# Kernel optimization log

Hardware: AMD Instinct MI355X
Metric: run time of the kernel (lower is better)

The kernel has to match this reference:

```python
import jax, jax.numpy as jnp
import numpy as np

D_IN = 1024
D_OUT = 1024
NUM_HEADS = 16
HEAD_DIM = D_OUT // NUM_HEADS
SCALE = HEAD_DIM ** -0.5


def setup_inputs() -> dict:
    key = jax.random.key(0)
    k_x, k_qkv, k_pw, k_pb = jax.random.split(key, 4)
    B, S = 2, 2048
    x = jax.random.normal(k_x, (B, S, D_IN), dtype=jnp.float32)
    # nn.Linear weights: stored as (out_features, in_features); qkv_bias=False
    w_qkv = jax.random.normal(k_qkv, (3 * D_OUT, D_IN), dtype=jnp.float32) * (D_IN ** -0.5)
    w_proj = jax.random.normal(k_pw, (D_OUT, D_OUT), dtype=jnp.float32) * (D_OUT ** -0.5)
    b_proj = jax.random.normal(k_pb, (D_OUT,), dtype=jnp.float32) * 0.01
    return {"x": x, "w_qkv": w_qkv, "w_proj": w_proj, "b_proj": b_proj}


def reference(x, w_qkv, w_proj, b_proj):
    B, S, _ = x.shape
    # combined QKV projection: (B,S,3*d_out)
    qkv = jnp.einsum('bsd,ed->bse', x, w_qkv)
    qkv = qkv.reshape(B, S, 3, NUM_HEADS, HEAD_DIM)
    qkv = jnp.transpose(qkv, (2, 0, 3, 1, 4))  # (3,B,H,S,hd)
    q, k, v = qkv[0], qkv[1], qkv[2]
    scores = jnp.einsum('bhqd,bhkd->bhqk', q, k)  # (B,H,S,S)
    causal = jnp.triu(jnp.ones((S, S), dtype=bool), k=1)
    # module masks to -inf first, then scales (softmax-equivalent)
    scores = jnp.where(causal, -jnp.inf, scores) * SCALE
    attn = jax.nn.softmax(scores, axis=-1)
    ctx = jnp.einsum('bhqk,bhkd->bhqd', attn, v)
    ctx = jnp.transpose(ctx, (0, 2, 1, 3)).reshape(B, S, D_OUT)
    return jnp.einsum('bsd,ed->bse', ctx, w_proj) + b_proj
```

## Files before the change

kernel.cpp:

```cpp
#include <hip/hip_runtime.h>

#define SEQ    2048
#define NHEAD  16
#define HDIM   64
#define DMODEL 1024
#define BATCH  2

typedef __bf16 bf16;
typedef __bf16 bf16x8 __attribute__((ext_vector_type(8)));
typedef __bf16 bf16x4v __attribute__((ext_vector_type(4)));
typedef float  f32x4  __attribute__((ext_vector_type(4)));

typedef const __attribute__((address_space(1))) void* gas_ptr;
typedef __attribute__((address_space(3))) void*       las_ptr;

__device__ __forceinline__ f32x4 mfma16(bf16x8 a, bf16x8 b, f32x4 c) {
  return __builtin_amdgcn_mfma_f32_16x16x32_bf16(a, b, c, 0, 0, 0);
}

__device__ __forceinline__ void gload_lds16(const void* g, void* l) {
  __builtin_amdgcn_global_load_lds((gas_ptr)(unsigned long long)g,
                                   (las_ptr)(unsigned long long)l, 16, 0, 0);
}

__global__ void convert_all(const float* __restrict__ x, const float* __restrict__ wq,
                            const float* __restrict__ wp, bf16* __restrict__ out) {
  const long long NX = 4194304, NQ = 3145728, NP = 1048576;
  long long i = ((long long)blockIdx.x * blockDim.x + threadIdx.x) * 4;
  if (i >= NX + NQ + NP) return;
  const float* src; long long off;
  if (i < NX)           { src = x;  off = i; }
  else if (i < NX + NQ) { src = wq; off = i - NX; }
  else                  { src = wp; off = i - NX - NQ; }
  float4 f = *reinterpret_cast<const float4*>(src + off);
  bf16x4v r;
  r[0] = (bf16)f.x; r[1] = (bf16)f.y; r[2] = (bf16)f.z; r[3] = (bf16)f.w;
  *reinterpret_cast<bf16x4v*>(out + i) = r;
}

template <int EPI>
__global__ __launch_bounds__(256) void gemm_bt(
    const bf16* __restrict__ A, const bf16* __restrict__ B, int K,
    bf16* __restrict__ q, bf16* __restrict__ k, bf16* __restrict__ v,
    const float* __restrict__ bias, float* __restrict__ out) {
  __shared__ alignas(16) bf16 As[2][128 * 32];
  __shared__ alignas(16) bf16 Bs[2][128 * 32];

  const int tid = threadIdx.x;
  const int l = tid & 63, w = tid >> 6;
  const int lr = l & 15, lg = l >> 4;
  const int wr = (w >> 1) * 64, wc = (w & 1) * 64;
  const long long m0 = (long long)blockIdx.x * 128;
  const long long n0 = (long long)blockIdx.y * 128;
  const int crow = tid >> 2, ccol = (tid & 3) * 8;

  auto stage = [&](int kt, int buf) {
    const bf16* a_src = A + (m0 + crow) * K + (long long)kt * 32 + ccol;
    const bf16* b_src = B + (n0 + crow) * K + (long long)kt * 32 + ccol;
    gload_lds16(a_src,           &As[buf][tid * 8]);
    gload_lds16(a_src + 64LL * K, &As[buf][(tid + 256) * 8]);
    gload_lds16(b_src,           &Bs[buf][tid * 8]);
    gload_lds16(b_src + 64LL * K, &Bs[buf][(tid + 256) * 8]);
  };

  f32x4 acc[4][4];
  const f32x4 fz = {0.f, 0.f, 0.f, 0.f};
#pragma unroll
  for (int m = 0; m < 4; ++m)
#pragma unroll
    for (int n = 0; n < 4; ++n) acc[m][n] = fz;

  stage(0, 0);
  const int nk = K >> 5;
  int cur = 0;
  for (int kt = 0; kt < nk; ++kt) {
    __syncthreads();
    if (kt + 1 < nk) stage(kt + 1, cur ^ 1);
    bf16x8 af[4], bfv[4];
#pragma unroll
    for (int m = 0; m < 4; ++m)
      af[m] = *reinterpret_cast<const bf16x8*>(&As[cur][(wr + m * 16 + lr) * 32 + lg * 8]);
#pragma unroll
    for (int n = 0; n < 4; ++n)
      bfv[n] = *reinterpret_cast<const bf16x8*>(&Bs[cur][(wc + n * 16 + lr) * 32 + lg * 8]);
#pragma unroll
    for (int m = 0; m < 4; ++m)
#pragma unroll
      for (int n = 0; n < 4; ++n) acc[m][n] = mfma16(af[m], bfv[n], acc[m][n]);
    cur ^= 1;
  }

#pragma unroll
  for (int m = 0; m < 4; ++m) {
#pragma unroll
    for (int n = 0; n < 4; ++n) {
#pragma unroll
      for (int j = 0; j < 4; ++j) {
        long long grow = m0 + wr + m * 16 + lg * 4 + j;
        long long gcol = n0 + wc + n * 16 + lr;
        float val = acc[m][n][j];
        if (EPI == 0) {
          int three = (int)(gcol >> 10);
          int rem = (int)(gcol & 1023);
          int h = rem >> 6, d = rem & 63;
          int b = (int)(grow >> 11), s = (int)(grow & 2047);
          int bh = b * NHEAD + h;
          if (three < 2) {
            int dst = ((bh * 128 + (s >> 4)) * 2 + (d >> 5)) * 512 +
                      (s & 15) * 8 + ((d >> 3) & 3) * 128 + (d & 7);
            if (three == 0) q[dst] = (bf16)(val * 0.18033688f);
            else            k[dst] = (bf16)val;
          } else {
            int dst = (((bh * 4 + (d >> 4)) * 32 + (s >> 6)) * 2 + ((s >> 5) & 1)) * 512 +
                      (d & 15) * 8 + ((s >> 3) & 3) * 128 + (s & 7);
            v[dst] = (bf16)val;
          }
        } else {
          out[grow * 1024 + gcol] = val + bias[gcol];
        }
      }
    }
  }
}

__global__ __launch_bounds__(256, 2) void attn_kernel(
    const bf16* __restrict__ qbuf, const bf16* __restrict__ kbuf,
    const bf16* __restrict__ vbuf, bf16* __restrict__ ctx) {
  const int lid = blockIdx.y * gridDim.x + blockIdx.x;
  const int xcd = lid & 7;
  const int idx = lid >> 3;
  const int bh  = xcd + (idx >> 4) * 8;
  const int p   = idx & 15;
  const int tid = threadIdx.x;
  const int l = tid & 63, w = tid >> 6;
  const int lr = l & 15, lg = l >> 4;
  const int loff = l * 8;

  __shared__ alignas(16) bf16 Ks[2][4096];
  __shared__ alignas(16) bf16 Vs[2][4096];
  __shared__ alignas(16) bf16 Pl[4][16][72];

  const bf16* Kg = kbuf + bh * 131072;
  const bf16* Vg = vbuf + bh * 131072;
  const int b = bh >> 4, h = bh & 15;
  const f32x4 fz = {0.f, 0.f, 0.f, 0.f};

  auto stage = [&](int kt, int sb) {
#pragma unroll
    for (int j = 0; j < 2; ++j) {
      const int c = 2 * w + j;
      gload_lds16(Kg + kt * 4096 + c * 512 + loff, &Ks[sb][c * 512 + loff]);
      gload_lds16(Vg + w * 32768 + kt * 1024 + j * 512 + loff, &Vs[sb][c * 512 + loff]);
    }
  };

  f32x4 o[4];
  float mrow[4], lsum[4];
  bf16x8 qf[2];

  stage(0, 0);
  __syncthreads();
  int buf = 0;

  for (int i = 0; i < 33; ++i) {
    const bool in_a = (i <= p);
    const int qt = in_a ? p : 31 - p;
    const int kt = in_a ? i : i - p - 1;
    const bool diag = (kt == qt);

    if (kt == 0) {
      const bf16* Qb = qbuf + (bh * 128 + qt * 4 + w) * 1024;
      qf[0] = *reinterpret_cast<const bf16x8*>(Qb + loff);
      qf[1] = *reinterpret_cast<const bf16x8*>(Qb + 512 + loff);
#pragma unroll
      for (int nd = 0; nd < 4; ++nd) o[nd] = fz;
#pragma unroll
      for (int j = 0; j < 4; ++j) { mrow[j] = -1e30f; lsum[j] = 0.f; }
    }

    if (i + 1 < 33) {
      const int i2 = i + 1;
      stage((i2 <= p) ? i2 : i2 - p - 1, buf ^ 1);
    }

    f32x4 s4[4];
#pragma unroll
    for (int n = 0; n < 4; ++n) {
      bf16x8 k0 = *reinterpret_cast<const bf16x8*>(&Ks[buf][(n * 2 + 0) * 512 + loff]);
      bf16x8 k1 = *reinterpret_cast<const bf16x8*>(&Ks[buf][(n * 2 + 1) * 512 + loff]);
      s4[n] = mfma16(qf[1], k1, mfma16(qf[0], k0, fz));
    }
    if (diag) {
#pragma unroll
      for (int n = 0; n < 4; ++n)
#pragma unroll
        for (int j = 0; j < 4; ++j)
          if (n * 16 + lr > w * 16 + lg * 4 + j) s4[n][j] = -1e30f;
    }

    float pm[4];
    float dmax = -1e30f;
#pragma unroll
    for (int j = 0; j < 4; ++j) {
      pm[j] = fmaxf(fmaxf(s4[0][j], s4[1][j]), fmaxf(s4[2][j], s4[3][j]));
      dmax = fmaxf(dmax, pm[j] - mrow[j]);
    }
    if (__any(dmax > 11.0f)) {
#pragma unroll
      for (int msk = 1; msk <= 8; msk <<= 1)
#pragma unroll
        for (int j = 0; j < 4; ++j) pm[j] = fmaxf(pm[j], __shfl_xor(pm[j], msk, 64));
#pragma unroll
      for (int j = 0; j < 4; ++j) {
        float mn = fmaxf(mrow[j], pm[j]);
        float alpha = exp2f(mrow[j] - mn);
        mrow[j] = mn;
        lsum[j] *= alpha;
#pragma unroll
        for (int nd = 0; nd < 4; ++nd) o[nd][j] *= alpha;
      }
    }

    float rs[4] = {0.f, 0.f, 0.f, 0.f};
#pragma unroll
    for (int n = 0; n < 4; ++n)
#pragma unroll
      for (int j = 0; j < 4; ++j) {
        float pv = exp2f(s4[n][j] - mrow[j]);
        s4[n][j] = pv;
        rs[j] += pv;
      }
#pragma unroll
    for (int j = 0; j < 4; ++j) lsum[j] += rs[j];

#pragma unroll
    for (int n = 0; n < 4; ++n)
#pragma unroll
      for (int j = 0; j < 4; ++j)
        Pl[w][lg * 4 + j][n * 16 + lr] = (bf16)s4[n][j];

#pragma unroll
    for (int kk = 0; kk < 2; ++kk) {
      bf16x8 pf = *reinterpret_cast<const bf16x8*>(&Pl[w][lr][kk * 32 + lg * 8]);
#pragma unroll
      for (int nd = 0; nd < 4; ++nd) {
        bf16x8 vfr = *reinterpret_cast<const bf16x8*>(&Vs[buf][(nd * 2 + kk) * 512 + loff]);
        o[nd] = mfma16(pf, vfr, o[nd]);
      }
    }

    if (diag) {
      float ls[4];
#pragma unroll
      for (int j = 0; j < 4; ++j) ls[j] = lsum[j];
#pragma unroll
      for (int msk = 1; msk <= 8; msk <<= 1)
#pragma unroll
        for (int j = 0; j < 4; ++j) ls[j] += __shfl_xor(ls[j], msk, 64);
      float inv[4];
#pragma unroll
      for (int j = 0; j < 4; ++j) inv[j] = 1.0f / ls[j];
      const int qr0 = (qt * 4 + w) * 16;
#pragma unroll
      for (int nd = 0; nd < 4; ++nd)
#pragma unroll
        for (int j = 0; j < 4; ++j) {
          int srow = qr0 + lg * 4 + j;
          int d = nd * 16 + lr;
          ctx[((long long)(b * SEQ + srow)) * DMODEL + h * HDIM + d] =
              (bf16)(o[nd][j] * inv[j]);
        }
    }

    __syncthreads();
    buf ^= 1;
  }
}

extern "C" void kernel_launch(void* const* d_in, const int* in_sizes, int n_in,
                              void* d_out, int out_size, void* d_ws, size_t ws_size,
                              hipStream_t stream) {
  const float* x      = (const float*)d_in[0];
  const float* w_qkv  = (const float*)d_in[1];
  const float* w_proj = (const float*)d_in[2];
  const float* b_proj = (const float*)d_in[3];
  float* out = (float*)d_out;

  bf16* ws = (bf16*)d_ws;
  bf16* xb     = ws;
  bf16* wqkvb  = xb + 4194304;
  bf16* wprojb = wqkvb + 3145728;
  bf16* qb     = wprojb + 1048576;
  bf16* kb     = qb + 4194304;
  bf16* vb     = kb + 4194304;
  bf16* ctxb   = vb + 4194304;

  convert_all<<<8192, 256, 0, stream>>>(x, w_qkv, w_proj, xb);
  gemm_bt<0><<<dim3(32, 24), 256, 0, stream>>>(xb, wqkvb, 1024, qb, kb, vb, nullptr, nullptr);
  attn_kernel<<<dim3(16, 32), 256, 0, stream>>>(qb, kb, vb, ctxb);
  gemm_bt<1><<<dim3(32, 8), 256, 0, stream>>>(ctxb, wprojb, 1024, nullptr, nullptr, nullptr,
                                              b_proj, out);
}
```

Before: 186.8 us.

## Process two KV tiles per barrier in attention; use narrower tiles for output projection

The attention kernel now stages two K/V tiles per buffer and processes a pair of tiles between barriers. This halves the number of __syncthreads and deepens the prefetch, at the cost of doubling LDS for K/V. The output-projection GEMM is templated to a 128x64 tile, giving 512 blocks instead of 256 and better fills the CUs. The trade-off is lower reuse of each A tile.

```diff
diff --git a/kernel.cpp b/kernel.cpp
--- a/kernel.cpp
+++ b/kernel.cpp
@@ -38,37 +38,39 @@
   *reinterpret_cast<bf16x4v*>(out + i) = r;
 }
 
-template <int EPI>
+template <int EPI, int BN>
 __global__ __launch_bounds__(256) void gemm_bt(
     const bf16* __restrict__ A, const bf16* __restrict__ B, int K,
     bf16* __restrict__ q, bf16* __restrict__ k, bf16* __restrict__ v,
     const float* __restrict__ bias, float* __restrict__ out) {
+  constexpr int NN = BN / 32;
   __shared__ alignas(16) bf16 As[2][128 * 32];
-  __shared__ alignas(16) bf16 Bs[2][128 * 32];
+  __shared__ alignas(16) bf16 Bs[2][BN * 32];
 
   const int tid = threadIdx.x;
   const int l = tid & 63, w = tid >> 6;
   const int lr = l & 15, lg = l >> 4;
-  const int wr = (w >> 1) * 64, wc = (w & 1) * 64;
+  const int wr = (w >> 1) * 64, wc = (w & 1) * (BN / 2);
   const long long m0 = (long long)blockIdx.x * 128;
-  const long long n0 = (long long)blockIdx.y * 128;
+  const long long n0 = (long long)blockIdx.y * BN;
   const int crow = tid >> 2, ccol = (tid & 3) * 8;
 
   auto stage = [&](int kt, int buf) {
     const bf16* a_src = A + (m0 + crow) * K + (long long)kt * 32 + ccol;
     const bf16* b_src = B + (n0 + crow) * K + (long long)kt * 32 + ccol;
-    gload_lds16(a_src,           &As[buf][tid * 8]);
+    gload_lds16(a_src,            &As[buf][tid * 8]);
     gload_lds16(a_src + 64LL * K, &As[buf][(tid + 256) * 8]);
-    gload_lds16(b_src,           &Bs[buf][tid * 8]);
-    gload_lds16(b_src + 64LL * K, &Bs[buf][(tid + 256) * 8]);
+    gload_lds16(b_src,            &Bs[buf][tid * 8]);
+    if constexpr (BN == 128)
+      gload_lds16(b_src + 64LL * K, &Bs[buf][(tid + 256) * 8]);
   };
 
-  f32x4 acc[4][4];
+  f32x4 acc[4][NN];
   const f32x4 fz = {0.f, 0.f, 0.f, 0.f};
 #pragma unroll
   for (int m = 0; m < 4; ++m)
 #pragma unroll
-    for (int n = 0; n < 4; ++n) acc[m][n] = fz;
+    for (int n = 0; n < NN; ++n) acc[m][n] = fz;
 
   stage(0, 0);
   const int nk = K >> 5;
@@ -76,24 +78,24 @@
   for (int kt = 0; kt < nk; ++kt) {
     __syncthreads();
     if (kt + 1 < nk) stage(kt + 1, cur ^ 1);
-    bf16x8 af[4], bfv[4];
+    bf16x8 af[4], bfv[NN];
 #pragma unroll
     for (int m = 0; m < 4; ++m)
       af[m] = *reinterpret_cast<const bf16x8*>(&As[cur][(wr + m * 16 + lr) * 32 + lg * 8]);
 #pragma unroll
-    for (int n = 0; n < 4; ++n)
+    for (int n = 0; n < NN; ++n)
       bfv[n] = *reinterpret_cast<const bf16x8*>(&Bs[cur][(wc + n * 16 + lr) * 32 + lg * 8]);
 #pragma unroll
     for (int m = 0; m < 4; ++m)
 #pragma unroll
-      for (int n = 0; n < 4; ++n) acc[m][n] = mfma16(af[m], bfv[n], acc[m][n]);
+      for (int n = 0; n < NN; ++n) acc[m][n] = mfma16(af[m], bfv[n], acc[m][n]);
     cur ^= 1;
   }
 
 #pragma unroll
   for (int m = 0; m < 4; ++m) {
 #pragma unroll
-    for (int n = 0; n < 4; ++n) {
+    for (int n = 0; n < NN; ++n) {
 #pragma unroll
       for (int j = 0; j < 4; ++j) {
         long long grow = m0 + wr + m * 16 + lg * 4 + j;
@@ -136,8 +138,8 @@
   const int lr = l & 15, lg = l >> 4;
   const int loff = l * 8;
 
-  __shared__ alignas(16) bf16 Ks[2][4096];
-  __shared__ alignas(16) bf16 Vs[2][4096];
+  __shared__ alignas(16) bf16 Ks[2][2][4096];
+  __shared__ alignas(16) bf16 Vs[2][2][4096];
   __shared__ alignas(16) bf16 Pl[4][16][72];
 
   const bf16* Kg = kbuf + bh * 131072;
@@ -145,24 +147,23 @@
   const int b = bh >> 4, h = bh & 15;
   const f32x4 fz = {0.f, 0.f, 0.f, 0.f};
 
-  auto stage = [&](int kt, int sb) {
-#pragma unroll
-    for (int j = 0; j < 2; ++j) {
-      const int c = 2 * w + j;
-      gload_lds16(Kg + kt * 4096 + c * 512 + loff, &Ks[sb][c * 512 + loff]);
-      gload_lds16(Vg + w * 32768 + kt * 1024 + j * 512 + loff, &Vs[sb][c * 512 + loff]);
-    }
-  };
-
   f32x4 o[4];
   float mrow[4], lsum[4];
   bf16x8 qf[2];
 
-  stage(0, 0);
-  __syncthreads();
-  int buf = 0;
-
-  for (int i = 0; i < 33; ++i) {
+  auto tile_kt = [&](int i) { return (i <= p) ? i : i - p - 1; };
+
+  auto stage_tile = [&](int i, int sb, int slot) {
+    const int kt = tile_kt(i);
+#pragma unroll
+    for (int j = 0; j < 2; ++j) {
+      const int c = 2 * w + j;
+      gload_lds16(Kg + kt * 4096 + c * 512 + loff, &Ks[sb][slot][c * 512 + loff]);
+      gload_lds16(Vg + w * 32768 + kt * 1024 + j * 512 + loff, &Vs[sb][slot][c * 512 + loff]);
+    }
+  };
+
+  auto process = [&](int i, int sb, int slot) {
     const bool in_a = (i <= p);
     const int qt = in_a ? p : 31 - p;
     const int kt = in_a ? i : i - p - 1;
@@ -178,16 +179,11 @@
       for (int j = 0; j < 4; ++j) { mrow[j] = -1e30f; lsum[j] = 0.f; }
     }
 
-    if (i + 1 < 33) {
-      const int i2 = i + 1;
-      stage((i2 <= p) ? i2 : i2 - p - 1, buf ^ 1);
-    }
-
     f32x4 s4[4];
 #pragma unroll
     for (int n = 0; n < 4; ++n) {
-      bf16x8 k0 = *reinterpret_cast<const bf16x8*>(&Ks[buf][(n * 2 + 0) * 512 + loff]);
-      bf16x8 k1 = *reinterpret_cast<const bf16x8*>(&Ks[buf][(n * 2 + 1) * 512 + loff]);
+      bf16x8 k0 = *reinterpret_cast<const bf16x8*>(&Ks[sb][slot][(n * 2 + 0) * 512 + loff]);
+      bf16x8 k1 = *reinterpret_cast<const bf16x8*>(&Ks[sb][slot][(n * 2 + 1) * 512 + loff]);
       s4[n] = mfma16(qf[1], k1, mfma16(qf[0], k0, fz));
     }
     if (diag) {
@@ -244,7 +240,7 @@
       bf16x8 pf = *reinterpret_cast<const bf16x8*>(&Pl[w][lr][kk * 32 + lg * 8]);
 #pragma unroll
       for (int nd = 0; nd < 4; ++nd) {
-        bf16x8 vfr = *reinterpret_cast<const bf16x8*>(&Vs[buf][(nd * 2 + kk) * 512 + loff]);
+        bf16x8 vfr = *reinterpret_cast<const bf16x8*>(&Vs[sb][slot][(nd * 2 + kk) * 512 + loff]);
         o[nd] = mfma16(pf, vfr, o[nd]);
       }
     }
@@ -271,7 +267,18 @@
               (bf16)(o[nd][j] * inv[j]);
         }
     }
-
+  };
+
+  stage_tile(0, 0, 0);
+  stage_tile(1, 0, 1);
+  __syncthreads();
+  int buf = 0;
+
+  for (int ip = 0; ip < 17; ++ip) {
+    if (2 * ip + 2 < 33) stage_tile(2 * ip + 2, buf ^ 1, 0);
+    if (2 * ip + 3 < 33) stage_tile(2 * ip + 3, buf ^ 1, 1);
+    process(2 * ip, buf, 0);
+    if (2 * ip + 1 < 33) process(2 * ip + 1, buf, 1);
     __syncthreads();
     buf ^= 1;
   }
@@ -296,8 +303,9 @@
   bf16* ctxb   = vb + 4194304;
 
   convert_all<<<8192, 256, 0, stream>>>(x, w_qkv, w_proj, xb);
-  gemm_bt<0><<<dim3(32, 24), 256, 0, stream>>>(xb, wqkvb, 1024, qb, kb, vb, nullptr, nullptr);
+  gemm_bt<0, 128><<<dim3(32, 24), 256, 0, stream>>>(xb, wqkvb, 1024, qb, kb, vb,
+                                                    nullptr, nullptr);
   attn_kernel<<<dim3(16, 32), 256, 0, stream>>>(qb, kb, vb, ctxb);
-  gemm_bt<1><<<dim3(32, 8), 256, 0, stream>>>(ctxb, wprojb, 1024, nullptr, nullptr, nullptr,
-                                              b_proj, out);
-}
+  gemm_bt<1, 64><<<dim3(32, 16), 256, 0, stream>>>(ctxb, wprojb, 1024, nullptr, nullptr,
+                                                   nullptr, b_proj, out);
+}
```

Result: no change. 185.0 us (-1.0%).
